# Performance work log

Measured on AMD Instinct MI355X. Metric: run time of the kernel, lower is better.

The kernel has to match this reference:

```python
import jax, jax.numpy as jnp
import numpy as np
from jax import lax

ALPHA = 0.3  # SSGConv alpha


def _cdist(x):
    # Euclidean distance matrix [N, N] for x: [N, H]
    n2 = jnp.sum(x * x, axis=-1)
    d2 = n2[:, None] + n2[None, :] - 2.0 * (x @ x.T)
    return jnp.sqrt(jnp.maximum(d2, 0.0))


def _prim(dist):
    # Dense O(N^2) Prim MST starting at node 0. Returns (parents, children, weights), each [N-1].
    N = dist.shape[0]
    INF = jnp.float32(1e30)
    in_tree = jnp.zeros(N, dtype=bool).at[0].set(True)
    mind = dist[0]                       # best edge weight into tree per node
    parent = jnp.zeros(N, dtype=jnp.int32)

    def step(carry, _):
        in_tree, mind, parent = carry
        d = jnp.where(in_tree, INF, mind)
        v = jnp.argmin(d).astype(jnp.int32)
        w = d[v]
        p = parent[v]
        in_tree = in_tree.at[v].set(True)
        newd = dist[v]
        upd = newd < mind
        mind = jnp.where(upd, newd, mind)
        parent = jnp.where(upd, v, parent)
        return (in_tree, mind, parent), (p, v, w)

    _, (ps, vs, ws) = lax.scan(step, (in_tree, mind, parent), None, length=N - 1)
    return ps, vs, ws


def _build_edges(features):
    # Torch code detaches edge weights via .item(); mirror with stop_gradient.
    B, N, _ = features.shape
    dist = jax.vmap(_cdist)(lax.stop_gradient(features))   # [B, N, N]
    ps, vs, ws = jax.vmap(_prim)(dist)                     # each [B, N-1]
    off = (jnp.arange(B, dtype=jnp.int32) * N)[:, None]
    a = (ps + off).ravel()
    b = (vs + off).ravel()
    src = jnp.concatenate([a, b])   # MST edges are added in both directions
    dst = jnp.concatenate([b, a])
    ew = jnp.concatenate([ws.ravel(), ws.ravel()])
    return src, dst, ew


def _gcn_norm(src, dst, ew, num_nodes):
    # PyG gcn_norm: add self loops (weight 1), symmetric deg^-1/2 normalization.
    loop = jnp.arange(num_nodes, dtype=src.dtype)
    src = jnp.concatenate([src, loop])
    dst = jnp.concatenate([dst, loop])
    ew = jnp.concatenate([ew, jnp.ones(num_nodes, ew.dtype)])
    deg = jax.ops.segment_sum(ew, dst, num_segments=num_nodes)
    dinv = jnp.where(deg > 0, lax.rsqrt(jnp.maximum(deg, 1e-30)), 0.0)
    norm = dinv[src] * ew * dinv[dst]
    return src, dst, norm


def _ssg_conv(x, src, dst, norm, W, b, num_nodes):
    # SSGConv with K=1: h = alpha*x + (1-alpha)*A_hat x, then linear.
    prop = jax.ops.segment_sum(norm[:, None] * x[src], dst, num_segments=num_nodes)
    h = ALPHA * x + (1.0 - ALPHA) * prop
    return h @ W + b


def _forward(features, W1, b1, W2, b2, W3, b3, Wd, bd, Wo, bo):
    B, N, H = features.shape
    NT = B * N
    src, dst, ew = _build_edges(features)
    src, dst, norm = _gcn_norm(src, dst, ew, NT)
    x = features.reshape(NT, H)
    x = jnp.tanh(_ssg_conv(x, src, dst, norm, W1, b1, NT))
    x = jnp.tanh(_ssg_conv(x, src, dst, norm, W2, b2, NT))
    x = jnp.tanh(_ssg_conv(x, src, dst, norm, W3, b3, NT))
    # dropout: eval mode -> identity. global_mean_pool: each graph has exactly N nodes.
    pooled = x.reshape(B, N, -1).mean(axis=1)          # [B, 2H]
    h = jnp.tanh(pooled @ Wd + bd)                     # [B, H]
    return h @ Wo + bo                                 # [B, num_labels]


def setup_inputs() -> dict:
    key = jax.random.key(0)
    ks = jax.random.split(key, 12)
    B, N, H, L = 16, 1024, 256, 8
    H2 = 2 * H

    def lin(k, fin, fout):
        s = 1.0 / np.sqrt(fin)
        k1, k2 = jax.random.split(k)
        return (jax.random.uniform(k1, (fin, fout), jnp.float32, -s, s),
                jax.random.uniform(k2, (fout,), jnp.float32, -s, s))

    W1, b1 = lin(ks[1], H, H2)
    W2, b2 = lin(ks[2], H2, H2)
    W3, b3 = lin(ks[3], H2, H2)
    Wd, bd = lin(ks[4], H2, H)
    Wo, bo = lin(ks[5], H, L)
    features = jax.random.normal(ks[0], (B, N, H), jnp.float32)
    return {"features": features, "W1": W1, "b1": b1, "W2": W2, "b2": b2,
            "W3": W3, "b3": b3, "Wd": Wd, "bd": bd, "Wo": Wo, "bo": bo}


def reference(features, W1, b1, W2, b2, W3, b3, Wd, bd, Wo, bo):
    return _forward(features, W1, b1, W2, b2, W3, b3, Wd, bd, Wo, bo)
```

## Files before the change

kernel.cpp:

```cpp
#include <hip/hip_runtime.h>
#include <math.h>

namespace {

constexpr float ALPHA = 0.3f;
constexpr int B  = 16;
constexpr int N  = 1024;
constexpr int H  = 256;
constexpr int H2 = 512;
constexpr int NT = B * N;
constexpr int NE = N - 1;
constexpr int CAP = 32;

__device__ __forceinline__ unsigned umin32(unsigned a, unsigned b) { return a < b ? a : b; }

typedef __attribute__((ext_vector_type(8))) short short8;
typedef __attribute__((ext_vector_type(4))) float f32x4;

__global__ void n2_kernel(const float* __restrict__ x, float* __restrict__ n2) {
  int wave = threadIdx.x >> 6, lane = threadIdx.x & 63;
  int row  = blockIdx.x * 4 + wave;
  float4 v = *(const float4*)(x + (size_t)row * H + lane * 4);
  float s  = v.x * v.x + v.y * v.y + v.z * v.z + v.w * v.w;
  #pragma unroll
  for (int off = 32; off; off >>= 1) s += __shfl_xor(s, off);
  if (lane == 0) n2[row] = s;
}

__global__ __launch_bounds__(256) void dist_kernel(const float* __restrict__ x,
    const float* __restrict__ n2, float* __restrict__ dist) {
  __shared__ float sh[128][136];
  const int bb = blockIdx.z;
  int idx = blockIdx.x, ti = 0;
  while (idx >= 8 - ti) { idx -= 8 - ti; ++ti; }
  const int tj = ti + idx;
  const int i0 = ti * 128, j0 = tj * 128;
  const int t = threadIdx.x, tx = t & 15, ty = t >> 4;
  const float* xb = x + (size_t)bb * N * H;
  float acc[8][8] = {};
  for (int kc = 0; kc < H; kc += 16) {
    #pragma unroll
    for (int u = 0; u < 2; ++u) {
      int q = t + u * 256;
      int row = q >> 2, kf = (q & 3) * 4;
      float4 a = *(const float4*)(xb + (size_t)(i0 + row) * H + kc + kf);
      sh[kf + 0][row] = a.x; sh[kf + 1][row] = a.y;
      sh[kf + 2][row] = a.z; sh[kf + 3][row] = a.w;
      float4 bv = *(const float4*)(xb + (size_t)(j0 + row) * H + kc + kf);
      sh[16 + kf + 0][row] = bv.x; sh[16 + kf + 1][row] = bv.y;
      sh[16 + kf + 2][row] = bv.z; sh[16 + kf + 3][row] = bv.w;
    }
    __syncthreads();
    #pragma unroll
    for (int kk = 0; kk < 16; ++kk) {
      float4 a0 = *(const float4*)&sh[kk][ty * 4];
      float4 a1 = *(const float4*)&sh[kk][64 + ty * 4];
      float4 b0 = *(const float4*)&sh[16 + kk][tx * 4];
      float4 b1 = *(const float4*)&sh[16 + kk][64 + tx * 4];
      float ar[8] = {a0.x,a0.y,a0.z,a0.w,a1.x,a1.y,a1.z,a1.w};
      float br[8] = {b0.x,b0.y,b0.z,b0.w,b1.x,b1.y,b1.z,b1.w};
      #pragma unroll
      for (int r = 0; r < 8; ++r)
        #pragma unroll
        for (int c = 0; c < 8; ++c) acc[r][c] += ar[r] * br[c];
    }
    __syncthreads();
  }
  float n2i[8], n2j[8];
  #pragma unroll
  for (int r = 0; r < 8; ++r)
    n2i[r] = n2[bb * N + i0 + (r < 4 ? ty * 4 + r : 64 + ty * 4 + r - 4)];
  #pragma unroll
  for (int c = 0; c < 8; ++c)
    n2j[c] = n2[bb * N + j0 + (c < 4 ? tx * 4 + c : 64 + tx * 4 + c - 4)];
  const bool mirror = (ti != tj);
  float* distb = dist + (size_t)bb * N * N;
  #pragma unroll
  for (int r = 0; r < 8; ++r) {
    int rl = (r < 4 ? ty * 4 + r : 64 + ty * 4 + r - 4);
    float o[8];
    #pragma unroll
    for (int c = 0; c < 8; ++c) {
      float d2 = (n2i[r] + n2j[c]) - 2.0f * acc[r][c];
      o[c] = sqrtf(fmaxf(d2, 0.0f));
    }
    float* dst = distb + (size_t)(i0 + rl) * N + j0;
    *(float4*)(dst + tx * 4)      = make_float4(o[0], o[1], o[2], o[3]);
    *(float4*)(dst + 64 + tx * 4) = make_float4(o[4], o[5], o[6], o[7]);
    if (mirror) {
      *(float4*)&sh[rl][tx * 4]      = make_float4(o[0], o[1], o[2], o[3]);
      *(float4*)&sh[rl][64 + tx * 4] = make_float4(o[4], o[5], o[6], o[7]);
    }
  }
  if (mirror) {
    __syncthreads();
    const int q = t >> 1, half = (t & 1) * 64;
    float* gdst = distb + (size_t)(j0 + q) * N + i0 + half;
    #pragma unroll
    for (int s = 0; s < 64; s += 4) {
      float4 v;
      v.x = sh[half + s + 0][q];
      v.y = sh[half + s + 1][q];
      v.z = sh[half + s + 2][q];
      v.w = sh[half + s + 3][q];
      *(float4*)(gdst + s) = v;
    }
  }
}

__device__ __forceinline__ unsigned wave_min_u32(unsigned x) {
  unsigned t;
  t = (unsigned)__builtin_amdgcn_update_dpp((int)x, (int)x, 0x111, 0xf, 0xf, false); x = umin32(x, t);
  t = (unsigned)__builtin_amdgcn_update_dpp((int)x, (int)x, 0x112, 0xf, 0xf, false); x = umin32(x, t);
  t = (unsigned)__builtin_amdgcn_update_dpp((int)x, (int)x, 0x114, 0xf, 0xf, false); x = umin32(x, t);
  t = (unsigned)__builtin_amdgcn_update_dpp((int)x, (int)x, 0x118, 0xf, 0xf, false); x = umin32(x, t);
  x = umin32(x, (unsigned)__shfl_xor((int)x, 16));
  x = umin32(x, (unsigned)__shfl_xor((int)x, 32));
  return (unsigned)__builtin_amdgcn_readlane((int)x, 63);
}

struct Sel2 { unsigned w; int j; };

__device__ __forceinline__ Sel2 block_select(unsigned mw0, unsigned mw1,
    unsigned mw2, unsigned mw3, int wid, int lane,
    unsigned long long (*smin)[4], int pb) {
  unsigned lm = umin32(umin32(mw0, mw1), umin32(mw2, mw3));
  unsigned wm = wave_min_u32(lm);
  unsigned mb = (mw0 == wm ? 1u : 0u) | (mw1 == wm ? 2u : 0u) |
                (mw2 == wm ? 4u : 0u) | (mw3 == wm ? 8u : 0u);
  unsigned long long bal = __ballot(mb != 0);
  int fl = __ffsll(bal) - 1;
  int slot = __ffs((unsigned)__builtin_amdgcn_readlane((int)mb, fl)) - 1;
  int widx = (wid << 8) | (fl << 2) | slot;
  if (lane == 0)
    smin[pb][wid] = ((unsigned long long)wm << 32) | (unsigned)widx;
  __syncthreads();
  unsigned long long k0 = smin[pb][0], k1 = smin[pb][1];
  unsigned long long k2 = smin[pb][2], k3 = smin[pb][3];
  unsigned long long ka = k0 < k1 ? k0 : k1;
  unsigned long long kb = k2 < k3 ? k2 : k3;
  unsigned long long kk = ka < kb ? ka : kb;
  Sel2 r; r.w = (unsigned)(kk >> 32); r.j = (int)(unsigned)(kk & 0xFFFFFFFFu);
  return r;
}

__global__ __launch_bounds__(256) void prim_gemm1_kernel(
    const float* __restrict__ dist, const float* __restrict__ feat,
    const float* __restrict__ W1, int* __restrict__ ep, int* __restrict__ ev,
    float* __restrict__ ewt, float* __restrict__ y) {
  __shared__ unsigned long long smin[2][4];
  __shared__ int epv[NE];
  __shared__ int evv[NE];
  __shared__ float ews[NE];
  __shared__ float As[16][132], Bs[16][132];
  if (blockIdx.x < B) {
    const int b = blockIdx.x;
    const int tid = threadIdx.x, wid = tid >> 6, lane = tid & 63;
    const float* Db = dist + (size_t)b * N * N;
    const int jbase = tid * 4;

    unsigned d0, d1, d2, d3;
    {
      float4 v = *(const float4*)(Db + jbase);
      d0 = __float_as_uint(v.x); d1 = __float_as_uint(v.y);
      d2 = __float_as_uint(v.z); d3 = __float_as_uint(v.w);
    }
    unsigned mw0 = d0, mw1 = d1, mw2 = d2, mw3 = d3;
    unsigned rm0 = 0, rm1 = 0, rm2 = 0, rm3 = 0;
    int pa0 = 0, pa1 = 0, pa2 = 0, pa3 = 0;
    if (tid == 0) { rm0 = ~0u; mw0 = ~0u; }

    Sel2 s0 = block_select(mw0, mw1, mw2, mw3, wid, lane, smin, 0);
    int cj = s0.j;
    if ((cj >> 2) == tid) {
      int sl = cj & 3;
      int pv = pa0; if (sl == 1) pv = pa1; if (sl == 2) pv = pa2; if (sl == 3) pv = pa3;
      epv[0] = pv; evv[0] = cj; ews[0] = __uint_as_float(s0.w);
      if (sl == 0) { rm0 = ~0u; mw0 = ~0u; }
      if (sl == 1) { rm1 = ~0u; mw1 = ~0u; }
      if (sl == 2) { rm2 = ~0u; mw2 = ~0u; }
      if (sl == 3) { rm3 = ~0u; mw3 = ~0u; }
    }
    float4 xq = *(const float4*)(Db + (size_t)cj * N + jbase);

    for (int k = 1; k < NE; ++k) {
      unsigned r0 = __float_as_uint(xq.x), r1 = __float_as_uint(xq.y);
      unsigned r2 = __float_as_uint(xq.z), r3 = __float_as_uint(xq.w);
      unsigned q0 = r0 | rm0, q1 = r1 | rm1, q2 = r2 | rm2, q3 = r3 | rm3;
      mw0 = umin32(mw0, q0); mw1 = umin32(mw1, q1);
      mw2 = umin32(mw2, q2); mw3 = umin32(mw3, q3);
      Sel2 se = block_select(mw0, mw1, mw2, mw3, wid, lane, smin, k & 1);
      const int nj = se.j;
      float4 nxt = *(const float4*)(Db + (size_t)nj * N + jbase);
      if (r0 < d0) { pa0 = cj; d0 = r0; }
      if (r1 < d1) { pa1 = cj; d1 = r1; }
      if (r2 < d2) { pa2 = cj; d2 = r2; }
      if (r3 < d3) { pa3 = cj; d3 = r3; }
      if ((nj >> 2) == tid) {
        int sl = nj & 3;
        int pv = pa0; if (sl == 1) pv = pa1; if (sl == 2) pv = pa2; if (sl == 3) pv = pa3;
        epv[k] = pv; evv[k] = nj; ews[k] = __uint_as_float(se.w);
        if (sl == 0) { rm0 = ~0u; mw0 = ~0u; }
        if (sl == 1) { rm1 = ~0u; mw1 = ~0u; }
        if (sl == 2) { rm2 = ~0u; mw2 = ~0u; }
        if (sl == 3) { rm3 = ~0u; mw3 = ~0u; }
      }
      cj = nj; xq = nxt;
    }

    __syncthreads();
    for (int e = tid; e < NE; e += 256) {
      ep[b * NE + e]  = epv[e];
      ev[b * NE + e]  = evv[e];
      ewt[b * NE + e] = ews[e];
    }
  } else {
    const int gb = blockIdx.x - B;
    const int m0 = (gb >> 2) * 128, n0 = (gb & 3) * 128;
    const int t = threadIdx.x, tx = t & 15, ty = t >> 4;
    float acc[8][8] = {};
    for (int kc = 0; kc < H; kc += 16) {
      #pragma unroll
      for (int u = 0; u < 2; ++u) {
        int q = t + u * 256;
        int row = q >> 2, kf = (q & 3) * 4;
        float4 a = *(const float4*)(feat + (size_t)(m0 + row) * H + kc + kf);
        As[kf + 0][row] = a.x; As[kf + 1][row] = a.y;
        As[kf + 2][row] = a.z; As[kf + 3][row] = a.w;
        int rowB = q >> 5, cf = (q & 31) * 4;
        *(float4*)&Bs[rowB][cf] = *(const float4*)(W1 + (size_t)(kc + rowB) * H2 + n0 + cf);
      }
      __syncthreads();
      #pragma unroll
      for (int kk = 0; kk < 16; ++kk) {
        float4 a0 = *(const float4*)&As[kk][ty * 4];
        float4 a1 = *(const float4*)&As[kk][64 + ty * 4];
        float4 b0 = *(const float4*)&Bs[kk][tx * 4];
        float4 b1 = *(const float4*)&Bs[kk][64 + tx * 4];
        float ar[8] = {a0.x,a0.y,a0.z,a0.w,a1.x,a1.y,a1.z,a1.w};
        float br[8] = {b0.x,b0.y,b0.z,b0.w,b1.x,b1.y,b1.z,b1.w};
        #pragma unroll
        for (int r = 0; r < 8; ++r)
          #pragma unroll
          for (int c = 0; c < 8; ++c) acc[r][c] += ar[r] * br[c];
      }
      __syncthreads();
    }
    #pragma unroll
    for (int r = 0; r < 8; ++r) {
      int m = m0 + (r < 4 ? ty * 4 + r : 64 + ty * 4 + r - 4);
      float* dst = y + (size_t)m * H2 + n0;
      *(float4*)(dst + tx * 4)      = make_float4(acc[r][0], acc[r][1], acc[r][2], acc[r][3]);
      *(float4*)(dst + 64 + tx * 4) = make_float4(acc[r][4], acc[r][5], acc[r][6], acc[r][7]);
    }
  }
}

__global__ void adj_kernel(const int* __restrict__ ep, const int* __restrict__ ev,
    const float* __restrict__ ewt, int* __restrict__ adjI, float* __restrict__ adjW,
    int* __restrict__ cnt, float* __restrict__ dinv) {
  int i = blockIdx.x * 256 + threadIdx.x;
  int b = i >> 10, loc = i & 1023;
  const int* epb = ep + b * NE;
  const int* evb = ev + b * NE;
  const float* ewb = ewt + b * NE;
  int c = 0; float wsum = 0.0f;
  for (int k = 0; k < NE; ++k) {
    int p = epb[k], v = evb[k];
    if (p == loc || v == loc) {
      float w = ewb[k];
      wsum += w;
      int nb = (p == loc) ? v : p;
      if (c < CAP) { adjI[i * CAP + c] = (b << 10) + nb; adjW[i * CAP + c] = w; }
      ++c;
    }
  }
  cnt[i]  = c < CAP ? c : CAP;
  dinv[i] = 1.0f / sqrtf(wsum + 1.0f);
}

__global__ void finish1_kernel(const float* __restrict__ y, const int* __restrict__ adjI,
    const float* __restrict__ adjW, const int* __restrict__ cnt,
    const float* __restrict__ dinv, const float* __restrict__ b1,
    float* __restrict__ out1) {
  int wave = threadIdx.x >> 6, lane = threadIdx.x & 63;
  int i = blockIdx.x * 4 + wave;
  float dv = dinv[i];
  int c = cnt[i];
  float selfc = ALPHA + (1.0f - ALPHA) * dv * dv;
  float4 acc[2];
  const float* yi = y + (size_t)i * H2 + lane * 4;
  #pragma unroll
  for (int u = 0; u < 2; ++u) {
    float4 v = *(const float4*)(yi + u * 256);
    acc[u].x = selfc * v.x; acc[u].y = selfc * v.y;
    acc[u].z = selfc * v.z; acc[u].w = selfc * v.w;
  }
  for (int e = 0; e < c; ++e) {
    int j   = adjI[i * CAP + e];
    float w = adjW[i * CAP + e];
    float coef = (1.0f - ALPHA) * dv * (w * dinv[j]);
    const float* yj = y + (size_t)j * H2 + lane * 4;
    #pragma unroll
    for (int u = 0; u < 2; ++u) {
      float4 v = *(const float4*)(yj + u * 256);
      acc[u].x += coef * v.x; acc[u].y += coef * v.y;
      acc[u].z += coef * v.z; acc[u].w += coef * v.w;
    }
  }
  float* ho = out1 + (size_t)i * H2 + lane * 4;
  #pragma unroll
  for (int u = 0; u < 2; ++u) {
    float4 bb = *(const float4*)(b1 + lane * 4 + u * 256);
    float4 o;
    o.x = tanhf(acc[u].x + bb.x); o.y = tanhf(acc[u].y + bb.y);
    o.z = tanhf(acc[u].z + bb.z); o.w = tanhf(acc[u].w + bb.w);
    *(float4*)(ho + u * 256) = o;
  }
}

template <int HH>
__global__ void prop_kernel(const float* __restrict__ x, const int* __restrict__ adjI,
    const float* __restrict__ adjW, const int* __restrict__ cnt,
    const float* __restrict__ dinv, float* __restrict__ h) {
  constexpr int U = HH / 256;
  int wave = threadIdx.x >> 6, lane = threadIdx.x & 63;
  int i = blockIdx.x * 4 + wave;
  float dv = dinv[i];
  int c = cnt[i];
  float selfc = ALPHA + (1.0f - ALPHA) * dv * dv;
  float4 acc[U];
  const float* xi = x + (size_t)i * HH + lane * 4;
  #pragma unroll
  for (int u = 0; u < U; ++u) {
    float4 v = *(const float4*)(xi + u * 256);
    acc[u].x = selfc * v.x; acc[u].y = selfc * v.y;
    acc[u].z = selfc * v.z; acc[u].w = selfc * v.w;
  }
  for (int e = 0; e < c; ++e) {
    int j   = adjI[i * CAP + e];
    float w = adjW[i * CAP + e];
    float coef = (1.0f - ALPHA) * dv * (w * dinv[j]);
    const float* xj = x + (size_t)j * HH + lane * 4;
    #pragma unroll
    for (int u = 0; u < U; ++u) {
      float4 v = *(const float4*)(xj + u * 256);
      acc[u].x += coef * v.x; acc[u].y += coef * v.y;
      acc[u].z += coef * v.z; acc[u].w += coef * v.w;
    }
  }
  float* ho = h + (size_t)i * HH + lane * 4;
  #pragma unroll
  for (int u = 0; u < U; ++u) *(float4*)(ho + u * 256) = acc[u];
}

__device__ __forceinline__ void bf16split(float a, unsigned short& hi, unsigned short& lo) {
  unsigned u = __float_as_uint(a);
  hi = (unsigned short)(u >> 16);
  float fh = __uint_as_float(u & 0xFFFF0000u);
  float fl = a - fh;
  lo = (unsigned short)(__float_as_uint(fl) >> 16);
}

__global__ __launch_bounds__(256) void mgemm_tanh_kernel(const float* __restrict__ A,
    const float* __restrict__ W, const float* __restrict__ bias, float* __restrict__ C) {
  __shared__ unsigned short Ahi[128][40], Alo[128][40];
  __shared__ unsigned short Bhi[128][40], Blo[128][40];
  const int m0 = blockIdx.x * 128, n0 = blockIdx.y * 128;
  const int t = threadIdx.x;
  const int w = t >> 6, lane = t & 63;
  const int lrow = lane & 15, lk = (lane >> 4) * 8;
  f32x4 acc[2][8];
  #pragma unroll
  for (int mt = 0; mt < 2; ++mt)
    #pragma unroll
    for (int nt = 0; nt < 8; ++nt) acc[mt][nt] = (f32x4){0.f, 0.f, 0.f, 0.f};

  const int arow = t >> 1, akq = (t & 1) * 16;
  const int wr = t & 31, wc4 = (t >> 5) * 16;

  for (int kc = 0; kc < H2; kc += 32) {
    {
      const float* src = A + (size_t)(m0 + arow) * H2 + kc + akq;
      unsigned short h[16], l[16];
      #pragma unroll
      for (int i = 0; i < 16; i += 4) {
        float4 v = *(const float4*)(src + i);
        bf16split(v.x, h[i], l[i]);     bf16split(v.y, h[i+1], l[i+1]);
        bf16split(v.z, h[i+2], l[i+2]); bf16split(v.w, h[i+3], l[i+3]);
      }
      short8 ph0 = {(short)h[0],(short)h[1],(short)h[2],(short)h[3],
                    (short)h[4],(short)h[5],(short)h[6],(short)h[7]};
      short8 ph1 = {(short)h[8],(short)h[9],(short)h[10],(short)h[11],
                    (short)h[12],(short)h[13],(short)h[14],(short)h[15]};
      short8 pl0 = {(short)l[0],(short)l[1],(short)l[2],(short)l[3],
                    (short)l[4],(short)l[5],(short)l[6],(short)l[7]};
      short8 pl1 = {(short)l[8],(short)l[9],(short)l[10],(short)l[11],
                    (short)l[12],(short)l[13],(short)l[14],(short)l[15]};
      *(short8*)&Ahi[arow][akq]     = ph0;
      *(short8*)&Ahi[arow][akq + 8] = ph1;
      *(short8*)&Alo[arow][akq]     = pl0;
      *(short8*)&Alo[arow][akq + 8] = pl1;
    }
    {
      const float* wsrc = W + (size_t)(kc + wr) * H2 + n0 + wc4;
      #pragma unroll
      for (int i = 0; i < 16; i += 4) {
        float4 v = *(const float4*)(wsrc + i);
        unsigned short h0,h1,h2,h3,l0,l1,l2,l3;
        bf16split(v.x, h0, l0); bf16split(v.y, h1, l1);
        bf16split(v.z, h2, l2); bf16split(v.w, h3, l3);
        Bhi[wc4+i+0][wr] = h0; Bhi[wc4+i+1][wr] = h1;
        Bhi[wc4+i+2][wr] = h2; Bhi[wc4+i+3][wr] = h3;
        Blo[wc4+i+0][wr] = l0; Blo[wc4+i+1][wr] = l1;
        Blo[wc4+i+2][wr] = l2; Blo[wc4+i+3][wr] = l3;
      }
    }
    __syncthreads();
    const int r0 = w * 32 + lrow;
    short8 a0h = *(const short8*)&Ahi[r0][lk];
    short8 a0l = *(const short8*)&Alo[r0][lk];
    short8 a1h = *(const short8*)&Ahi[r0 + 16][lk];
    short8 a1l = *(const short8*)&Alo[r0 + 16][lk];
    #pragma unroll
    for (int nt = 0; nt < 8; ++nt) {
      short8 bh = *(const short8*)&Bhi[nt * 16 + lrow][lk];
      short8 bl = *(const short8*)&Blo[nt * 16 + lrow][lk];
      acc[0][nt] = __builtin_amdgcn_mfma_f32_16x16x32_bf16(a0h, bh, acc[0][nt], 0, 0, 0);
      acc[0][nt] = __builtin_amdgcn_mfma_f32_16x16x32_bf16(a0l, bh, acc[0][nt], 0, 0, 0);
      acc[0][nt] = __builtin_amdgcn_mfma_f32_16x16x32_bf16(a0h, bl, acc[0][nt], 0, 0, 0);
      acc[1][nt] = __builtin_amdgcn_mfma_f32_16x16x32_bf16(a1h, bh, acc[1][nt], 0, 0, 0);
      acc[1][nt] = __builtin_amdgcn_mfma_f32_16x16x32_bf16(a1l, bh, acc[1][nt], 0, 0, 0);
      acc[1][nt] = __builtin_amdgcn_mfma_f32_16x16x32_bf16(a1h, bl, acc[1][nt], 0, 0, 0);
    }
    __syncthreads();
  }
  #pragma unroll
  for (int mt = 0; mt < 2; ++mt) {
    #pragma unroll
    for (int nt = 0; nt < 8; ++nt) {
      int col = n0 + nt * 16 + lrow;
      float bcol = bias[col];
      #pragma unroll
      for (int i = 0; i < 4; ++i) {
        int row = m0 + w * 32 + mt * 16 + (lane >> 4) * 4 + i;
        C[(size_t)row * H2 + col] = tanhf(acc[mt][nt][i] + bcol);
      }
    }
  }
}

__global__ void pool_head_kernel(const float* __restrict__ x,
    const float* __restrict__ Wd, const float* __restrict__ bd,
    const float* __restrict__ Wo, const float* __restrict__ bo,
    float* __restrict__ out) {
  __shared__ float sp[512], shh[256];
  int b = blockIdx.x, t = threadIdx.x;
  const float* xb = x + ((size_t)b << 10) * H2;
  float s0 = 0.0f, s1 = 0.0f;
  for (int i = 0; i < N; ++i) {
    s0 += xb[(size_t)i * H2 + t];
    s1 += xb[(size_t)i * H2 + t + 256];
  }
  sp[t] = s0 * (1.0f / N);
  sp[t + 256] = s1 * (1.0f / N);
  __syncthreads();
  float acc = bd[t];
  for (int c2 = 0; c2 < 512; ++c2) acc += sp[c2] * Wd[c2 * 256 + t];
  shh[t] = tanhf(acc);
  __syncthreads();
  if (t < 8) {
    float o = bo[t];
    for (int j = 0; j < 256; ++j) o += shh[j] * Wo[j * 8 + t];
    out[b * 8 + t] = o;
  }
}

}

extern "C" void kernel_launch(void* const* d_in, const int* in_sizes, int n_in,
                              void* d_out, int out_size, void* d_ws, size_t ws_size,
                              hipStream_t stream) {
  const float* feat = (const float*)d_in[0];
  const float* W1 = (const float*)d_in[1];
  const float* b1 = (const float*)d_in[2];
  const float* W2 = (const float*)d_in[3];
  const float* b2 = (const float*)d_in[4];
  const float* W3 = (const float*)d_in[5];
  const float* b3 = (const float*)d_in[6];
  const float* Wd = (const float*)d_in[7];
  const float* bd = (const float*)d_in[8];
  const float* Wo = (const float*)d_in[9];
  const float* bo = (const float*)d_in[10];
  float* out = (float*)d_out;
  char* ws = (char*)d_ws;

  float* dist = (float*)(ws);
  float* out1 = (float*)(ws);
  float* x2   = (float*)(ws + ((size_t)32 << 20));
  float* x3   = (float*)(ws);
  float* ybuf = (float*)(ws + ((size_t)64 << 20));
  float* hbuf = (float*)(ws + ((size_t)64 << 20));
  char* misc  = ws + ((size_t)96 << 20);
  int*   ep     = (int*)(misc);
  int*   ev     = (int*)(misc + 65536);
  float* ewt    = (float*)(misc + 131072);
  int*   cnt    = (int*)(misc + 196608);
  float* dinv   = (float*)(misc + 262144);
  int*   adjI   = (int*)(misc + 327680);
  float* adjW   = (float*)(misc + 327680 + 2097152);
  float* n2     = (float*)(misc + 327680 + 2 * 2097152);

  n2_kernel<<<NT / 4, 256, 0, stream>>>(feat, n2);
  dist_kernel<<<dim3(36, 1, 16), 256, 0, stream>>>(feat, n2, dist);
  prim_gemm1_kernel<<<B + (NT / 128) * 4, 256, 0, stream>>>(
      dist, feat, W1, ep, ev, ewt, ybuf);
  adj_kernel<<<NT / 256, 256, 0, stream>>>(ep, ev, ewt, adjI, adjW, cnt, dinv);

  finish1_kernel<<<NT / 4, 256, 0, stream>>>(ybuf, adjI, adjW, cnt, dinv, b1, out1);
  prop_kernel<512><<<NT / 4, 256, 0, stream>>>(out1, adjI, adjW, cnt, dinv, hbuf);
  mgemm_tanh_kernel<<<dim3(NT / 128, 4), 256, 0, stream>>>(hbuf, W2, b2, x2);
  prop_kernel<512><<<NT / 4, 256, 0, stream>>>(x2, adjI, adjW, cnt, dinv, hbuf);
  mgemm_tanh_kernel<<<dim3(NT / 128, 4), 256, 0, stream>>>(hbuf, W3, b3, x3);

  pool_head_kernel<<<B, 256, 0, stream>>>(x3, Wd, bd, Wo, bo, out);
}
```

Before: 1.115 ms.

## Add cache-warming blocks that stream each graph's distance matrix during Prim

Launches B extra blocks in the fused Prim/GEMM1 kernel. Each one repeatedly reads its graph's 4 MB distance matrix to keep it resident in cache while the serial Prim block runs, and stops once that graph's Prim block sets a completion flag. The flags are zeroed in n2_kernel. The aim is to cut the latency of Prim's row fetches, at the cost of extra memory traffic that competes with the GEMM blocks and of relying on volatile flag polling.

New measurement: 1.052 ms. -5.6%, faster.

```diff
diff --git a/kernel.cpp b/kernel.cpp
--- a/kernel.cpp
+++ b/kernel.cpp
@@ -11,13 +11,16 @@
 constexpr int NT = B * N;
 constexpr int NE = N - 1;
 constexpr int CAP = 32;
+constexpr int GEMM1_BLKS = (NT / 128) * 4;
 
 __device__ __forceinline__ unsigned umin32(unsigned a, unsigned b) { return a < b ? a : b; }
 
 typedef __attribute__((ext_vector_type(8))) short short8;
 typedef __attribute__((ext_vector_type(4))) float f32x4;
 
-__global__ void n2_kernel(const float* __restrict__ x, float* __restrict__ n2) {
+__global__ void n2_kernel(const float* __restrict__ x, float* __restrict__ n2,
+                          int* __restrict__ flags) {
+  if (blockIdx.x == 0 && threadIdx.x < B) flags[threadIdx.x] = 0;
   int wave = threadIdx.x >> 6, lane = threadIdx.x & 63;
   int row  = blockIdx.x * 4 + wave;
   float4 v = *(const float4*)(x + (size_t)row * H + lane * 4);
@@ -147,7 +150,7 @@
 __global__ __launch_bounds__(256) void prim_gemm1_kernel(
     const float* __restrict__ dist, const float* __restrict__ feat,
     const float* __restrict__ W1, int* __restrict__ ep, int* __restrict__ ev,
-    float* __restrict__ ewt, float* __restrict__ y) {
+    float* __restrict__ ewt, float* __restrict__ y, int* __restrict__ flags) {
   __shared__ unsigned long long smin[2][4];
   __shared__ int epv[NE];
   __shared__ int evv[NE];
@@ -214,7 +217,8 @@
       ev[b * NE + e]  = evv[e];
       ewt[b * NE + e] = ews[e];
     }
-  } else {
+    if (tid == 0) atomicExch(&flags[b], 1);
+  } else if (blockIdx.x < B + GEMM1_BLKS) {
     const int gb = blockIdx.x - B;
     const int m0 = (gb >> 2) * 128, n0 = (gb & 3) * 128;
     const int t = threadIdx.x, tx = t & 15, ty = t >> 4;
@@ -252,6 +256,24 @@
       float* dst = y + (size_t)m * H2 + n0;
       *(float4*)(dst + tx * 4)      = make_float4(acc[r][0], acc[r][1], acc[r][2], acc[r][3]);
       *(float4*)(dst + 64 + tx * 4) = make_float4(acc[r][4], acc[r][5], acc[r][6], acc[r][7]);
+    }
+  } else {
+    const int wb = blockIdx.x - (B + GEMM1_BLKS);
+    const float* Dw = dist + (size_t)wb * N * N;
+    volatile const int* flag = flags + wb;
+    const int t = threadIdx.x;
+    for (int pass = 0; pass < 16; ++pass) {
+      if (*flag != 0) break;
+      for (int off = 0; off < N * N; off += 16384) {
+        if (*flag != 0) break;
+        float s = 0.0f;
+        #pragma unroll
+        for (int q = 0; q < 16; ++q) {
+          float4 vv = *(const float4*)(Dw + off + q * 1024 + t * 4);
+          s += vv.x + vv.y + vv.z + vv.w;
+        }
+        asm volatile("" :: "v"(s));
+      }
     }
   }
 }
@@ -510,11 +532,12 @@
   int*   adjI   = (int*)(misc + 327680);
   float* adjW   = (float*)(misc + 327680 + 2097152);
   float* n2     = (float*)(misc + 327680 + 2 * 2097152);
-
-  n2_kernel<<<NT / 4, 256, 0, stream>>>(feat, n2);
+  int*   flags  = (int*)(misc + 327680 + 2 * 2097152 + 65536);
+
+  n2_kernel<<<NT / 4, 256, 0, stream>>>(feat, n2, flags);
   dist_kernel<<<dim3(36, 1, 16), 256, 0, stream>>>(feat, n2, dist);
-  prim_gemm1_kernel<<<B + (NT / 128) * 4, 256, 0, stream>>>(
-      dist, feat, W1, ep, ev, ewt, ybuf);
+  prim_gemm1_kernel<<<B + GEMM1_BLKS + B, 256, 0, stream>>>(
+      dist, feat, W1, ep, ev, ewt, ybuf, flags);
   adj_kernel<<<NT / 256, 256, 0, stream>>>(ep, ev, ewt, adjI, adjW, cnt, dinv);
 
   finish1_kernel<<<NT / 4, 256, 0, stream>>>(ybuf, adjI, adjW, cnt, dinv, b1, out1);
```
